# Performance work log

Measured on AMD Instinct MI355X. Metric: run time of the kernel, lower is better.

## Reference

```python
import jax, jax.numpy as jnp
import numpy as np

B, N, DIM = 4, 2048, 1024
H, DH = 16, 64


def setup_inputs() -> dict:
    key = jax.random.key(0)
    k1, k2, k3 = jax.random.split(key, 3)
    x = jax.random.normal(k1, (B, N, DIM), dtype=jnp.float32)
    # nn.Linear weight layout: [out_features, in_features]; y = x @ W.T
    w_qkv = jax.random.normal(k2, (3 * H * DH, DIM), dtype=jnp.float32) * (DIM ** -0.5)
    w_out = jax.random.normal(k3, (DIM, H * DH), dtype=jnp.float32) * ((H * DH) ** -0.5)
    b_out = jnp.zeros((DIM,), dtype=jnp.float32)
    return {"x": x, "w_qkv": w_qkv, "w_out": w_out, "b_out": b_out}


def reference(x, w_qkv, w_out, b_out):
    scale = DH ** -0.5
    qkv = jnp.einsum('bnd,ed->bne', x, w_qkv)            # [B,N,3*H*DH]
    q, k, v = jnp.split(qkv, 3, axis=-1)
    def to_heads(t):
        return t.reshape(B, N, H, DH).transpose(0, 2, 1, 3)  # b h n d
    q, k, v = to_heads(q), to_heads(k), to_heads(v)
    scores = jnp.einsum('bhnd,bhmd->bhnm', q, k) * scale  # [B,H,N,N]
    att = jax.nn.softmax(scores, axis=-1)
    out = jnp.einsum('bhnm,bhmd->bhnd', att, v)
    out = out.transpose(0, 2, 1, 3).reshape(B, N, H * DH)  # b n (h d)
    return jnp.einsum('bne,de->bnd', out, w_out) + b_out
```

## Files before the change

### kernel.cpp

```cpp
#include <hip/hip_runtime.h>
#include <hip/hip_bf16.h>
#include <math.h>

#define B_   4
#define N_   2048
#define DIM_ 1024
#define H_   16
#define DH_  64
#define E3_  3072

typedef __attribute__((ext_vector_type(8)))  short s8v;
typedef __attribute__((ext_vector_type(4)))  float f4v;
typedef __attribute__((ext_vector_type(16))) float f16v;

__device__ __forceinline__ unsigned short f2bf_fast(float f) {
    return (unsigned short)((__builtin_bit_cast(unsigned int, f) + 0x8000u) >> 16);
}
__device__ __forceinline__ unsigned int pkbf(float a, float b) {
    unsigned int ua = __builtin_bit_cast(unsigned int, a) + 0x8000u;
    unsigned int ub = __builtin_bit_cast(unsigned int, b) + 0x8000u;
    return __builtin_amdgcn_perm(ub, ua, 0x07060302);
}
__device__ __forceinline__ unsigned int cvtpk(float a, float b) {
    unsigned int r;
    asm("v_cvt_pk_bf16_f32 %0, %1, %2" : "=v"(r) : "v"(a), "v"(b));
    return r;
}
__device__ __forceinline__ uint2 pl32(unsigned int a, unsigned int b) {
    asm volatile("v_permlane32_swap_b32 %0, %1" : "+v"(a), "+v"(b));
    return make_uint2(a, b);
}

__device__ __forceinline__ void gload_lds16(const void* g, void* l) {
    __builtin_amdgcn_global_load_lds(
        (const __attribute__((address_space(1))) unsigned int*)(uintptr_t)g,
        (__attribute__((address_space(3))) unsigned int*)(uintptr_t)l,
        16, 0, 0);
}

__global__ __launch_bounds__(256) void cvt_bf16(
    const float* __restrict__ in, unsigned short* __restrict__ out, int n)
{
    const int i = (blockIdx.x * 256 + threadIdx.x) * 4;
    if (i < n) {
        float4 v = *(const float4*)(in + i);
        uint2 pk;
        pk.x = pkbf(v.x, v.y);
        pk.y = pkbf(v.z, v.w);
        *(uint2*)(out + i) = pk;
    }
}

template<int MODE>
__global__ __launch_bounds__(256) void gemm_mfma(
    const unsigned short* __restrict__ A,
    const unsigned short* __restrict__ Bw,
    const float* __restrict__ bias,
    unsigned short* __restrict__ Cb,
    unsigned short* __restrict__ Vt,
    float* __restrict__ Cf,
    int M, int Nc, int K)
{
    __shared__ unsigned short As[128 * 32];
    __shared__ unsigned short Bs[128 * 32];

    const int tid  = threadIdx.x;
    const int w    = tid >> 6;
    const int lane = tid & 63;
    const int quad = lane >> 4;
    const int l15  = lane & 15;
    const int wm   = w & 1, wn = w >> 1;

    const int nwx = gridDim.x;
    const int lin = blockIdx.y * nwx + blockIdx.x;
    const int cpx = (nwx * gridDim.y) >> 3;
    const int swz = (lin & 7) * cpx + (lin >> 3);
    const int m0  = (swz / nwx) * 128, n0 = (swz % nwx) * 128;

    const int srow = lane >> 2;
    const int sch  = (lane & 3) * 8;

    f4v acc[4][4];
    #pragma unroll
    for (int i = 0; i < 4; i++)
        #pragma unroll
        for (int j = 0; j < 4; j++) acc[i][j] = (f4v){0.f, 0.f, 0.f, 0.f};

    for (int k0 = 0; k0 < K; k0 += 32) {
        __syncthreads();
        #pragma unroll
        for (int i = 0; i < 2; i++) {
            const int rbase = w * 32 + i * 16;
            gload_lds16(A  + (size_t)(m0 + rbase + srow) * K + k0 + sch,
                        &As[rbase * 32]);
            gload_lds16(Bw + (size_t)(n0 + rbase + srow) * K + k0 + sch,
                        &Bs[rbase * 32]);
        }
        __syncthreads();

        s8v af[4], bf[4];
        #pragma unroll
        for (int i = 0; i < 4; i++) {
            af[i] = *(const s8v*)&As[(wm * 64 + i * 16 + l15) * 32 + quad * 8];
            bf[i] = *(const s8v*)&Bs[(wn * 64 + i * 16 + l15) * 32 + quad * 8];
        }
        #pragma unroll
        for (int ms = 0; ms < 4; ms++)
            #pragma unroll
            for (int ns = 0; ns < 4; ns++)
                acc[ms][ns] = __builtin_amdgcn_mfma_f32_16x16x32_bf16(
                    af[ms], bf[ns], acc[ms][ns], 0, 0, 0);
    }

    if (MODE == 0) {
        #pragma unroll
        for (int ns = 0; ns < 4; ns++) {
            const int colb = n0 + wn * 64 + ns * 16;
            if (colb < 2048) {
                const float mul = (colb < 1024) ? 0.18033688011112042f : 1.0f;
                #pragma unroll
                for (int ms = 0; ms < 4; ms++)
                    #pragma unroll
                    for (int r = 0; r < 4; r++) {
                        const int row = m0 + wm * 64 + ms * 16 + quad * 4 + r;
                        Cb[(size_t)row * Nc + colb + l15] = f2bf_fast(acc[ms][ns][r] * mul);
                    }
            } else {
                const int e = colb + l15 - 2048;
                const int h = e >> 6, d = e & 63;
                #pragma unroll
                for (int ms = 0; ms < 4; ms++) {
                    const int row = m0 + wm * 64 + ms * 16 + quad * 4;
                    const int b = row >> 11, n = row & 2047;
                    uint2 pk;
                    pk.x = pkbf(acc[ms][ns][0], acc[ms][ns][1]);
                    pk.y = pkbf(acc[ms][ns][2], acc[ms][ns][3]);
                    *(uint2*)&Vt[(((size_t)b * 16 + h) * 64 + d) * 2048 + n] = pk;
                }
            }
        }
    } else {
        #pragma unroll
        for (int ns = 0; ns < 4; ns++) {
            const float bz = bias[n0 + wn * 64 + ns * 16 + l15];
            #pragma unroll
            for (int ms = 0; ms < 4; ms++)
                #pragma unroll
                for (int r = 0; r < 4; r++) {
                    const int row = m0 + wm * 64 + ms * 16 + quad * 4 + r;
                    Cf[(size_t)row * Nc + n0 + wn * 64 + ns * 16 + l15] =
                        acc[ms][ns][r] + bz;
                }
        }
    }
}

__global__ __launch_bounds__(512, 4) void attn_mfma(
    const unsigned short* __restrict__ qkv,
    const unsigned short* __restrict__ vT,
    unsigned short* __restrict__ ao)
{
    __shared__ __align__(16) unsigned short Ks[2][64][64];
    __shared__ __align__(16) unsigned short Vs[2][64][64];

    const int tid  = threadIdx.x;
    const int w    = tid >> 6;
    const int lane = tid & 63;
    const int l31  = lane & 31;
    const int hi5  = lane >> 5;
    const int h8   = hi5 * 8;

    const int lin = blockIdx.y * 8 + blockIdx.x;
    const int swz = (lin & 7) * 64 + (lin >> 3);
    const int bx  = swz & 7;
    const int bh  = swz >> 3;
    const int b   = bh >> 4;
    const int h   = bh & 15;
    const int q0  = bx * 256;
    const int qb  = q0 + w * 32;

    const unsigned short* qp  = qkv + (size_t)b * N_ * E3_ + (size_t)h * DH_;
    const unsigned short* kp  = qp + 1024;
    const unsigned short* vtp = vT + (size_t)bh * 64 * 2048;

    const int drow = lane >> 3;
    const int dchk = (lane & 7) ^ drow;
    const int grow = w * 8 + drow;

    s8v bq[4];
    {
        const unsigned short* qrow = qp + (size_t)(qb + l31) * E3_;
        #pragma unroll
        for (int ks = 0; ks < 4; ks++)
            bq[ks] = *(const s8v*)(qrow + ks * 16 + h8);
    }

    s8v ones;
    #pragma unroll
    for (int i = 0; i < 8; i++) ones[i] = (short)0x3F80;

    const f16v fzero = {0.f,0.f,0.f,0.f,0.f,0.f,0.f,0.f,
                        0.f,0.f,0.f,0.f,0.f,0.f,0.f,0.f};
    f16v o0 = fzero, o1 = fzero;
    f16v lc = fzero;

    gload_lds16(kp  + (size_t)grow * E3_  + dchk * 8, &Ks[0][w * 8][0]);
    gload_lds16(vtp + (size_t)grow * 2048 + dchk * 8, &Vs[0][w * 8][0]);
    __syncthreads();

    for (int kt = 0; kt < N_ / 64; kt++) {
        const int cur = kt & 1;

        if (kt + 1 < N_ / 64) {
            const int kn = (kt + 1) * 64;
            gload_lds16(kp  + (size_t)(kn + grow) * E3_  + dchk * 8,
                        &Ks[cur ^ 1][w * 8][0]);
            gload_lds16(vtp + (size_t)grow * 2048 + kn + dchk * 8,
                        &Vs[cur ^ 1][w * 8][0]);
        }

        #pragma unroll
        for (int ksub = 0; ksub < 2; ksub++) {
            const int krow = ksub * 32 + l31;
            const int ksw  = (l31 & 7) * 8;
            s8v ak[4];
            #pragma unroll
            for (int ks = 0; ks < 4; ks++)
                ak[ks] = *(const s8v*)&Ks[cur][krow][(ks * 16 + h8) ^ ksw];

            f16v st = fzero;
            __builtin_amdgcn_s_setprio(1);
            st = __builtin_amdgcn_mfma_f32_32x32x16_bf16(ak[0], bq[0], st, 0, 0, 0);
            st = __builtin_amdgcn_mfma_f32_32x32x16_bf16(ak[1], bq[1], st, 0, 0, 0);
            st = __builtin_amdgcn_mfma_f32_32x32x16_bf16(ak[2], bq[2], st, 0, 0, 0);
            st = __builtin_amdgcn_mfma_f32_32x32x16_bf16(ak[3], bq[3], st, 0, 0, 0);
            __builtin_amdgcn_s_setprio(0);

            float pe[16];
            #pragma unroll
            for (int i = 0; i < 16; i++)
                pe[i] = __builtin_amdgcn_exp2f(st[i]);

            s8v pa[2];
            {
                union { s8v v; unsigned int u[4]; } f0, f1;
                uint2 r;
                r = pl32(cvtpk(pe[0],  pe[1]),  cvtpk(pe[4],  pe[5]));
                f0.u[0] = r.x; f0.u[2] = r.y;
                r = pl32(cvtpk(pe[2],  pe[3]),  cvtpk(pe[6],  pe[7]));
                f0.u[1] = r.x; f0.u[3] = r.y;
                r = pl32(cvtpk(pe[8],  pe[9]),  cvtpk(pe[12], pe[13]));
                f1.u[0] = r.x; f1.u[2] = r.y;
                r = pl32(cvtpk(pe[10], pe[11]), cvtpk(pe[14], pe[15]));
                f1.u[1] = r.x; f1.u[3] = r.y;
                pa[0] = f0.v;
                pa[1] = f1.v;
            }

            #pragma unroll
            for (int j = 0; j < 2; j++) {
                const int kbase = (ksub * 2 + j) * 16 + h8;
                const int vsw   = (l31 & 7) * 8;
                s8v bv0 = *(const s8v*)&Vs[cur][l31     ][kbase ^ vsw];
                s8v bv1 = *(const s8v*)&Vs[cur][32 + l31][kbase ^ vsw];
                __builtin_amdgcn_s_setprio(1);
                o0 = __builtin_amdgcn_mfma_f32_32x32x16_bf16(pa[j], bv0, o0, 0, 0, 0);
                o1 = __builtin_amdgcn_mfma_f32_32x32x16_bf16(pa[j], bv1, o1, 0, 0, 0);
                lc = __builtin_amdgcn_mfma_f32_32x32x16_bf16(pa[j], ones, lc, 0, 0, 0);
                __builtin_amdgcn_s_setprio(0);
            }
        }

        __syncthreads();
    }

    {
        float inv[16];
        #pragma unroll
        for (int r = 0; r < 16; r++) inv[r] = 1.f / lc[r];
        #pragma unroll
        for (int r = 0; r < 16; r++) {
            const int qrow = qb + (r & 3) + 8 * (r >> 2) + 4 * hi5;
            const size_t base = ((size_t)b * N_ + qrow) * (H_ * DH_) + h * DH_;
            ao[base + l31]      = f2bf_fast(o0[r] * inv[r]);
            ao[base + 32 + l31] = f2bf_fast(o1[r] * inv[r]);
        }
    }
}

extern "C" void kernel_launch(void* const* d_in, const int* in_sizes, int n_in,
                              void* d_out, int out_size, void* d_ws, size_t ws_size,
                              hipStream_t stream) {
    const float* x     = (const float*)d_in[0];
    const float* w_qkv = (const float*)d_in[1];
    const float* w_out = (const float*)d_in[2];
    const float* b_out = (const float*)d_in[3];
    float* out = (float*)d_out;

    char* ws = (char*)d_ws;
    unsigned short* x_bf    = (unsigned short*)(ws);
    unsigned short* wqkv_bf = (unsigned short*)(ws + (((size_t)16) << 20));
    unsigned short* wout_bf = (unsigned short*)(ws + (((size_t)22) << 20));
    unsigned short* qkv_bf  = (unsigned short*)(ws + (((size_t)24) << 20));
    unsigned short* vT      = (unsigned short*)(ws + (((size_t)72) << 20));
    unsigned short* ao_bf   = (unsigned short*)(ws + (((size_t)88) << 20));

    const int M = B_ * N_;

    cvt_bf16<<<(M * DIM_) / 1024, 256, 0, stream>>>(x, x_bf, M * DIM_);
    cvt_bf16<<<(E3_ * DIM_) / 1024, 256, 0, stream>>>(w_qkv, wqkv_bf, E3_ * DIM_);
    cvt_bf16<<<(DIM_ * DIM_) / 1024, 256, 0, stream>>>(w_out, wout_bf, DIM_ * DIM_);

    {
        dim3 grid(E3_ / 128, M / 128);
        gemm_mfma<0><<<grid, 256, 0, stream>>>(x_bf, wqkv_bf, nullptr,
                                               qkv_bf, vT, nullptr, M, E3_, DIM_);
    }
    {
        dim3 grid(N_ / 256, B_ * H_);
        attn_mfma<<<grid, 512, 0, stream>>>(qkv_bf, vT, ao_bf);
    }
    {
        dim3 grid(DIM_ / 128, M / 128);
        gemm_mfma<1><<<grid, 256, 0, stream>>>(ao_bf, wout_bf, b_out,
                                               nullptr, nullptr, out, M, DIM_, DIM_);
    }
    (void)in_sizes; (void)n_in; (void)out_size; (void)ws_size;
}
```

Measured before the change: 276.3 us.

## Specialize QKV GEMM with larger swizzled double-buffered LDS tiles

```diff
diff --git a/kernel.cpp b/kernel.cpp
--- a/kernel.cpp
+++ b/kernel.cpp
@@ -51,13 +51,119 @@
     }
 }
 
-template<int MODE>
-__global__ __launch_bounds__(256) void gemm_mfma(
+__global__ __launch_bounds__(512, 1) void gemm_qkv(
+    const unsigned short* __restrict__ A,
+    const unsigned short* __restrict__ Bw,
+    unsigned short* __restrict__ Cb,
+    unsigned short* __restrict__ Vt)
+{
+    __shared__ unsigned short Ls[2][28672];
+
+    const int tid  = threadIdx.x;
+    const int w    = tid >> 6;
+    const int lane = tid & 63;
+    const int quad = lane >> 4;
+    const int l15  = lane & 15;
+    const int wm   = w & 1;
+    const int wn   = w >> 1;
+
+    const int lin = blockIdx.y * 16 + blockIdx.x;
+    const int swz = (lin & 7) * 64 + (lin >> 3);
+    const int m0  = (swz >> 4) * 256;
+    const int n0  = (swz & 15) * 192;
+
+    const int r8  = lane >> 3;
+    const int chk = (lane & 7) ^ r8;
+
+    f4v acc[8][3];
+    #pragma unroll
+    for (int i = 0; i < 8; i++)
+        #pragma unroll
+        for (int j = 0; j < 3; j++) acc[i][j] = (f4v){0.f, 0.f, 0.f, 0.f};
+
+    #pragma unroll
+    for (int j = 0; j < 7; j++) {
+        const int u = w * 7 + j;
+        const unsigned short* src = (u < 32)
+            ? A  + (size_t)(m0 + u * 8 + r8) * 1024 + chk * 8
+            : Bw + (size_t)(n0 + (u - 32) * 8 + r8) * 1024 + chk * 8;
+        gload_lds16(src, &Ls[0][u * 512]);
+    }
+    __syncthreads();
+
+    for (int t = 0; t < 16; t++) {
+        const int cur = t & 1;
+
+        if (t + 1 < 16) {
+            const int k0 = (t + 1) * 64;
+            #pragma unroll
+            for (int j = 0; j < 7; j++) {
+                const int u = w * 7 + j;
+                const unsigned short* src = (u < 32)
+                    ? A  + (size_t)(m0 + u * 8 + r8) * 1024 + k0 + chk * 8
+                    : Bw + (size_t)(n0 + (u - 32) * 8 + r8) * 1024 + k0 + chk * 8;
+                gload_lds16(src, &Ls[cur ^ 1][u * 512]);
+            }
+        }
+
+        #pragma unroll
+        for (int s = 0; s < 2; s++) {
+            s8v af[8], bf[3];
+            #pragma unroll
+            for (int ms = 0; ms < 8; ms++) {
+                const int row = wm * 128 + ms * 16 + l15;
+                af[ms] = *(const s8v*)&Ls[cur][row * 64 + (((s * 4 + quad) ^ (l15 & 7)) * 8)];
+            }
+            #pragma unroll
+            for (int ns = 0; ns < 3; ns++) {
+                const int row = 256 + wn * 48 + ns * 16 + l15;
+                bf[ns] = *(const s8v*)&Ls[cur][row * 64 + (((s * 4 + quad) ^ (l15 & 7)) * 8)];
+            }
+            __builtin_amdgcn_s_setprio(1);
+            #pragma unroll
+            for (int ms = 0; ms < 8; ms++)
+                #pragma unroll
+                for (int ns = 0; ns < 3; ns++)
+                    acc[ms][ns] = __builtin_amdgcn_mfma_f32_16x16x32_bf16(
+                        af[ms], bf[ns], acc[ms][ns], 0, 0, 0);
+            __builtin_amdgcn_s_setprio(0);
+        }
+
+        __syncthreads();
+    }
+
+    #pragma unroll
+    for (int ns = 0; ns < 3; ns++) {
+        const int colb = n0 + wn * 48 + ns * 16;
+        if (colb < 2048) {
+            const float mul = (colb < 1024) ? 0.18033688011112042f : 1.0f;
+            #pragma unroll
+            for (int ms = 0; ms < 8; ms++)
+                #pragma unroll
+                for (int r = 0; r < 4; r++) {
+                    const int row = m0 + wm * 128 + ms * 16 + quad * 4 + r;
+                    Cb[(size_t)row * E3_ + colb + l15] = f2bf_fast(acc[ms][ns][r] * mul);
+                }
+        } else {
+            const int e = colb + l15 - 2048;
+            const int hh = e >> 6, d = e & 63;
+            #pragma unroll
+            for (int ms = 0; ms < 8; ms++) {
+                const int row = m0 + wm * 128 + ms * 16 + quad * 4;
+                const int bb = row >> 11, nn = row & 2047;
+                uint2 pk;
+                pk.x = pkbf(acc[ms][ns][0], acc[ms][ns][1]);
+                pk.y = pkbf(acc[ms][ns][2], acc[ms][ns][3]);
+                *(uint2*)&Vt[(((size_t)bb * 16 + hh) * 64 + d) * 2048 + nn] = pk;
+            }
+        }
+    }
+}
+
+__global__ __launch_bounds__(256) void gemm_out(
     const unsigned short* __restrict__ A,
     const unsigned short* __restrict__ Bw,
     const float* __restrict__ bias,
-    unsigned short* __restrict__ Cb,
-    unsigned short* __restrict__ Vt,
     float* __restrict__ Cf,
     int M, int Nc, int K)
 {
@@ -112,46 +218,17 @@
                     af[ms], bf[ns], acc[ms][ns], 0, 0, 0);
     }
 
-    if (MODE == 0) {
-        #pragma unroll
-        for (int ns = 0; ns < 4; ns++) {
-            const int colb = n0 + wn * 64 + ns * 16;
-            if (colb < 2048) {
-                const float mul = (colb < 1024) ? 0.18033688011112042f : 1.0f;
-                #pragma unroll
-                for (int ms = 0; ms < 4; ms++)
-                    #pragma unroll
-                    for (int r = 0; r < 4; r++) {
-                        const int row = m0 + wm * 64 + ms * 16 + quad * 4 + r;
-                        Cb[(size_t)row * Nc + colb + l15] = f2bf_fast(acc[ms][ns][r] * mul);
-                    }
-            } else {
-                const int e = colb + l15 - 2048;
-                const int h = e >> 6, d = e & 63;
-                #pragma unroll
-                for (int ms = 0; ms < 4; ms++) {
-                    const int row = m0 + wm * 64 + ms * 16 + quad * 4;
-                    const int b = row >> 11, n = row & 2047;
-                    uint2 pk;
-                    pk.x = pkbf(acc[ms][ns][0], acc[ms][ns][1]);
-                    pk.y = pkbf(acc[ms][ns][2], acc[ms][ns][3]);
-                    *(uint2*)&Vt[(((size_t)b * 16 + h) * 64 + d) * 2048 + n] = pk;
-                }
-            }
-        }
-    } else {
-        #pragma unroll
-        for (int ns = 0; ns < 4; ns++) {
-            const float bz = bias[n0 + wn * 64 + ns * 16 + l15];
-            #pragma unroll
-            for (int ms = 0; ms < 4; ms++)
-                #pragma unroll
-                for (int r = 0; r < 4; r++) {
-                    const int row = m0 + wm * 64 + ms * 16 + quad * 4 + r;
-                    Cf[(size_t)row * Nc + n0 + wn * 64 + ns * 16 + l15] =
-                        acc[ms][ns][r] + bz;
-                }
-        }
+    #pragma unroll
+    for (int ns = 0; ns < 4; ns++) {
+        const float bz = bias[n0 + wn * 64 + ns * 16 + l15];
+        #pragma unroll
+        for (int ms = 0; ms < 4; ms++)
+            #pragma unroll
+            for (int r = 0; r < 4; r++) {
+                const int row = m0 + wm * 64 + ms * 16 + quad * 4 + r;
+                Cf[(size_t)row * Nc + n0 + wn * 64 + ns * 16 + l15] =
+                    acc[ms][ns][r] + bz;
+            }
     }
 }
 
@@ -312,9 +389,8 @@
     cvt_bf16<<<(DIM_ * DIM_) / 1024, 256, 0, stream>>>(w_out, wout_bf, DIM_ * DIM_);
 
     {
-        dim3 grid(E3_ / 128, M / 128);
-        gemm_mfma<0><<<grid, 256, 0, stream>>>(x_bf, wqkv_bf, nullptr,
-                                               qkv_bf, vT, nullptr, M, E3_, DIM_);
+        dim3 grid(E3_ / 192, M / 256);
+        gemm_qkv<<<grid, 512, 0, stream>>>(x_bf, wqkv_bf, qkv_bf, vT);
     }
     {
         dim3 grid(N_ / 256, B_ * H_);
@@ -322,8 +398,8 @@
     }
     {
         dim3 grid(DIM_ / 128, M / 128);
-        gemm_mfma<1><<<grid, 256, 0, stream>>>(ao_bf, wout_bf, b_out,
-                                               nullptr, nullptr, out, M, DIM_, DIM_);
+        gemm_out<<<grid, 256, 0, stream>>>(ao_bf, wout_bf, b_out,
+                                           out, M, DIM_, DIM_);
     }
     (void)in_sizes; (void)n_in; (void)out_size; (void)ws_size;
 }
```

After: 257.7 us. 1.07x faster.
